# Kernel tuning notes

Measured on AMD Instinct MI355X. Metric: run time of the kernel, lower is better.

## Reference

```python
import jax, jax.numpy as jnp
import numpy as np

NUM_FEATURES = 256
NUM_PIDS = 5532
NUM_CQ = 5000
OIM_SCALAR = 30.0
IGNORE_INDEX = 5554  # roi_label 5555 -> label 5554 -> ignored by cross_entropy
N = 8192
UNLABELED_FRAC = 0.3


def _l2norm(x):
    return x / jnp.linalg.norm(x, axis=-1, keepdims=True)


def setup_inputs() -> dict:
    key = jax.random.key(0)
    k1, k2, k3, k4, k5 = jax.random.split(key, 5)
    inputs = _l2norm(jax.random.normal(k1, (N, NUM_FEATURES), dtype=jnp.float32))
    # roi_label values are 1..num_pids for labeled persons, 5555 for unlabeled;
    # all >= 1 so the `label >= 0` filter in the torch module keeps every row
    # (keeps shapes static / jit-friendly while matching the math exactly).
    labels = jax.random.randint(k2, (N,), 1, NUM_PIDS + 1, dtype=jnp.int32)
    unlabeled = jax.random.uniform(k3, (N,)) < UNLABELED_FRAC
    roi_label = jnp.where(unlabeled, IGNORE_INDEX + 1, labels).astype(jnp.int32)
    lut = _l2norm(jax.random.normal(k4, (NUM_PIDS, NUM_FEATURES), dtype=jnp.float32))
    cq = _l2norm(jax.random.normal(k5, (NUM_CQ, NUM_FEATURES), dtype=jnp.float32))
    return {"inputs": inputs, "roi_label": roi_label, "lut": lut, "cq": cq}


def reference(inputs, roi_label, lut, cq):
    # targets = cat(roi_label); label = targets - 1; inds = label >= 0 keeps all rows here
    label = roi_label - 1  # [N], values in [0, NUM_PIDS-1] or IGNORE_INDEX
    # OIMSMR.forward: projected = [inputs @ lut.T | inputs @ cq.T]
    logits = jnp.concatenate([inputs @ lut.T, inputs @ cq.T], axis=1)  # [N, P+Q]
    logits = logits * OIM_SCALAR
    # cross_entropy with ignore_index=5554 (mean over non-ignored samples)
    valid = label != IGNORE_INDEX
    safe_label = jnp.clip(label, 0, logits.shape[1] - 1)
    logp = jax.nn.log_softmax(logits, axis=1)  # [N, P+Q]
    nll = -jnp.take_along_axis(logp, safe_label[:, None], axis=1)[:, 0]  # [N]
    n_valid = jnp.maximum(jnp.sum(valid.astype(jnp.float32)), 1.0)
    loss = jnp.sum(jnp.where(valid, nll, 0.0)) / n_valid
    return loss
```

## Files before the change

kernel.cpp:

```cpp
#include <hip/hip_runtime.h>
#include <hip/hip_bf16.h>
#include <cstdint>
#include <cstddef>

#define N_ROWS 8192
#define K_DIM  256
#define NP     5532
#define NC     10532
#define NCPAD  10752
#define IGN    5554
#define BM     128
#define BN     128
#define BK     128
#define CT     84
#define NBLK   (CT * 64)
#define CPX    (NBLK / 8)
#define WSCALE 43.2808512266689f
#define LN2    0.69314718055994531f

#if __has_builtin(__builtin_amdgcn_exp2f)
#define EXP2F(x) __builtin_amdgcn_exp2f(x)
#else
#define EXP2F(x) __expf((x) * LN2)
#endif

using f32x4 = __attribute__((ext_vector_type(4))) float;
using i64x2 = __attribute__((ext_vector_type(2))) long;

__global__ __launch_bounds__(256) void oim_convert(
    const float* __restrict__ X, const float* __restrict__ lut,
    const float* __restrict__ cq,
    unsigned char* __restrict__ Xb, unsigned char* __restrict__ Wb)
{
    const int XCH = (N_ROWS * K_DIM) / 8;
    const int WCH = (NCPAD * K_DIM) / 8;
    int c = blockIdx.x * 256 + threadIdx.x;
    if (c >= XCH + WCH) return;
    const float* src = nullptr;
    unsigned char* dst;
    float scale = 1.0f;
    int row, qg;
    if (c < XCH) {
        row = c >> 5; qg = c & 31;
        src = X + (size_t)c * 8;
        dst = Xb + (size_t)row * K_DIM;
    } else {
        int wc = c - XCH;
        row = wc >> 5; qg = wc & 31;
        dst = Wb + (size_t)row * K_DIM;
        scale = WSCALE;
        if (row < NP)      src = lut + (size_t)row * K_DIM + qg * 8;
        else if (row < NC) src = cq + (size_t)(row - NP) * K_DIM + qg * 8;
    }
    dst += (qg >> 3) * 64 + (qg & 3) * 16 + ((qg >> 2) & 1) * 8;
    unsigned int lo = 0, hi = 0;
    if (src) {
        float4 v0 = *reinterpret_cast<const float4*>(src);
        float4 v1 = *reinterpret_cast<const float4*>(src + 4);
        lo = __builtin_amdgcn_cvt_pk_fp8_f32(v0.x * scale, v0.y * scale, 0,  false);
        lo = __builtin_amdgcn_cvt_pk_fp8_f32(v0.z * scale, v0.w * scale, lo, true);
        hi = __builtin_amdgcn_cvt_pk_fp8_f32(v1.x * scale, v1.y * scale, 0,  false);
        hi = __builtin_amdgcn_cvt_pk_fp8_f32(v1.z * scale, v1.w * scale, hi, true);
    }
    uint2 o; o.x = lo; o.y = hi;
    *reinterpret_cast<uint2*>(dst) = o;
}

__global__ __launch_bounds__(256, 3) void oim_gemm(
    const unsigned char* __restrict__ Xb, const unsigned char* __restrict__ Wb,
    const int* __restrict__ roi,
    float* __restrict__ partial, float* __restrict__ labelLogit)
{
    const int bid = blockIdx.x;
    const int L   = (bid & 7) * CPX + (bid >> 3);
    const int ct  = L >> 6;
    const int rt  = L & 63;
    const int row0 = rt * BM;
    const int col0 = ct * BN;
    const int tid  = threadIdx.x;
    const int wave = tid >> 6;
    const int lane = tid & 63;
    const int wm   = (wave >> 1) * 64;
    const int wn   = (wave & 1) * 64;

    __shared__ __align__(16) unsigned char As[BM * BK];
    __shared__ __align__(16) unsigned char Bs[BN * BK];
    __shared__ int   lbl[BM];
    __shared__ float rs[BM][2];

    if (tid < BM) lbl[tid] = roi[row0 + tid] - 1;

    const unsigned char* aP[4];
    const unsigned char* bP[4];
#pragma unroll
    for (int i = 0; i < 4; ++i) {
        int c = i * 256 + tid;
        int r = c >> 3;
        int u = c & 7;
        int s = ((u ^ (r & 7)) << 4);
        aP[i] = Xb + (size_t)(row0 + r) * K_DIM + s;
        bP[i] = Wb + (size_t)(col0 + r) * K_DIM + s;
    }

    const int rA = wm + (lane & 15);
    const int rB = wn + (lane & 15);
    const int gs = lane >> 4;
    int aO[2], bO[2];
#pragma unroll
    for (int kb = 0; kb < 2; ++kb) {
        aO[kb] = rA * 128 + (((kb * 4 + gs) ^ (rA & 7)) << 4);
        bO[kb] = rB * 128 + (((kb * 4 + gs) ^ (rB & 7)) << 4);
    }

    f32x4 acc[4][4] = {};
    long xa0[4], xa1[4], xb0[4], xb1[4];

    auto readfrag = [&](int kb) {
#pragma unroll
        for (int m = 0; m < 4; ++m) {
            i64x2 v = *reinterpret_cast<const i64x2*>(As + aO[kb] + m * 2048);
            xa0[m] = v.x; xa1[m] = v.y;
        }
#pragma unroll
        for (int n = 0; n < 4; ++n) {
            i64x2 v = *reinterpret_cast<const i64x2*>(Bs + bO[kb] + n * 2048);
            xb0[n] = v.x; xb1[n] = v.y;
        }
    };
    auto mfmafrag = [&]() {
#pragma unroll
        for (int m = 0; m < 4; ++m)
#pragma unroll
            for (int n = 0; n < 4; ++n)
                acc[m][n] = __builtin_amdgcn_mfma_f32_16x16x32_fp8_fp8(
                    xa0[m], xb0[n], acc[m][n], 0, 0, 0);
#pragma unroll
        for (int m = 0; m < 4; ++m)
#pragma unroll
            for (int n = 0; n < 4; ++n)
                acc[m][n] = __builtin_amdgcn_mfma_f32_16x16x32_fp8_fp8(
                    xa1[m], xb1[n], acc[m][n], 0, 0, 0);
    };

#define STAGE(T)                                                              \
    do {                                                                      \
        _Pragma("unroll")                                                     \
        for (int i = 0; i < 4; ++i) {                                         \
            __builtin_amdgcn_global_load_lds(                                 \
                (const __attribute__((address_space(1))) void*)aP[i],         \
                (__attribute__((address_space(3))) void*)                     \
                    ((char*)As + i * 4096 + wave * 1024), 16, (T) * 128, 0);  \
            __builtin_amdgcn_global_load_lds(                                 \
                (const __attribute__((address_space(1))) void*)bP[i],         \
                (__attribute__((address_space(3))) void*)                     \
                    ((char*)Bs + i * 4096 + wave * 1024), 16, (T) * 128, 0);  \
        }                                                                     \
    } while (0)

    STAGE(0);
    __syncthreads();

    readfrag(0); mfmafrag();
    readfrag(1);
    __syncthreads();
    STAGE(1);
    mfmafrag();
    __syncthreads();

    readfrag(0); mfmafrag();
    readfrag(1); mfmafrag();
#undef STAGE

#pragma unroll
    for (int m = 0; m < 4; ++m) {
#pragma unroll
        for (int reg = 0; reg < 4; ++reg) {
            int lrow = wm + m * 16 + (lane >> 4) * 4 + reg;
            int grow = row0 + lrow;
            int lab  = lbl[lrow];
            float s = 0.0f;
#pragma unroll
            for (int n = 0; n < 4; ++n) {
                int gcol = col0 + wn + n * 16 + (lane & 15);
                float a = acc[m][n][reg];
                s += EXP2F(a);
                if (gcol == lab) labelLogit[grow] = a;
            }
#pragma unroll
            for (int off = 1; off < 16; off <<= 1) s += __shfl_xor(s, off, 64);
            if ((lane & 15) == 0) rs[lrow][wave & 1] = s;
        }
    }
    __syncthreads();
    if (tid < BM)
        partial[(size_t)ct * N_ROWS + row0 + tid] = rs[tid][0] + rs[tid][1];
}

__global__ __launch_bounds__(256) void oim_rownll(
    const float* __restrict__ partial, const float* __restrict__ labelLogit,
    const int* __restrict__ roi, float* __restrict__ blksum)
{
    __shared__ float s1[256], s2[256];
    int tid = threadIdx.x;
    int r = blockIdx.x * 256 + tid;
    float S = 0.0f;
    for (int t = 0; t < CT; ++t) S += partial[(size_t)t * N_ROWS + r];
    float lse = logf(S);
    int lab = roi[r] - 1;
    bool valid = (lab != IGN);
    s1[tid] = valid ? (lse - labelLogit[r] * LN2) : 0.0f;
    s2[tid] = valid ? 1.0f : 0.0f;
    __syncthreads();
    for (int o = 128; o > 0; o >>= 1) {
        if (tid < o) { s1[tid] += s1[tid + o]; s2[tid] += s2[tid + o]; }
        __syncthreads();
    }
    if (tid == 0) {
        blksum[blockIdx.x]      = s1[0];
        blksum[32 + blockIdx.x] = s2[0];
    }
}

__global__ __launch_bounds__(64) void oim_reduce(
    const float* __restrict__ blksum, float* __restrict__ out)
{
    int tid = threadIdx.x;
    float a = (tid < 32) ? blksum[tid]      : 0.0f;
    float b = (tid < 32) ? blksum[32 + tid] : 0.0f;
#pragma unroll
    for (int off = 32; off > 0; off >>= 1) {
        a += __shfl_xor(a, off, 64);
        b += __shfl_xor(b, off, 64);
    }
    if (tid == 0) out[0] = a / fmaxf(b, 1.0f);
}

extern "C" void kernel_launch(void* const* d_in, const int* in_sizes, int n_in,
                              void* d_out, int out_size, void* d_ws, size_t ws_size,
                              hipStream_t stream)
{
    const float* X   = (const float*)d_in[0];
    const int*   roi = (const int*)  d_in[1];
    const float* lut = (const float*)d_in[2];
    const float* cq  = (const float*)d_in[3];
    float* out = (float*)d_out;

    char* ws = (char*)d_ws;
    unsigned char* Xb = (unsigned char*)ws;
    unsigned char* Wb = Xb + (size_t)N_ROWS * K_DIM;
    float* partial    = (float*)(Wb + (size_t)NCPAD * K_DIM);
    float* labelLogit = partial + (size_t)CT * N_ROWS;
    float* blksum     = labelLogit + N_ROWS;
    size_t need = (size_t)N_ROWS * K_DIM + (size_t)NCPAD * K_DIM
                + (size_t)CT * N_ROWS * 4 + (size_t)(N_ROWS + 64) * 4;
    if (ws_size < need) return;

    const int TOT_CHUNKS = ((N_ROWS + NCPAD) * K_DIM) / 8;
    oim_convert<<<(TOT_CHUNKS + 255) / 256, 256, 0, stream>>>(X, lut, cq, Xb, Wb);
    oim_gemm<<<NBLK, 256, 0, stream>>>(Xb, Wb, roi, partial, labelLogit);
    oim_rownll<<<N_ROWS / 256, 256, 0, stream>>>(partial, labelLogit, roi, blksum);
    oim_reduce<<<1, 64, 0, stream>>>(blksum, out);
}
```

Baseline: 63.17 us.

## Load full K=256 tile into LDS at once instead of two K-halves

New measurement: 84.69 us. 34.1% more time.

```diff
diff --git a/kernel.cpp b/kernel.cpp
--- a/kernel.cpp
+++ b/kernel.cpp
@@ -11,7 +11,6 @@
 #define IGN    5554
 #define BM     128
 #define BN     128
-#define BK     128
 #define CT     84
 #define NBLK   (CT * 64)
 #define CPX    (NBLK / 8)
@@ -66,7 +65,7 @@
     *reinterpret_cast<uint2*>(dst) = o;
 }
 
-__global__ __launch_bounds__(256, 3) void oim_gemm(
+__global__ __launch_bounds__(256, 2) void oim_gemm(
     const unsigned char* __restrict__ Xb, const unsigned char* __restrict__ Wb,
     const int* __restrict__ roi,
     float* __restrict__ partial, float* __restrict__ labelLogit)
@@ -83,51 +82,56 @@
     const int wm   = (wave >> 1) * 64;
     const int wn   = (wave & 1) * 64;
 
-    __shared__ __align__(16) unsigned char As[BM * BK];
-    __shared__ __align__(16) unsigned char Bs[BN * BK];
+    __shared__ __align__(16) unsigned char As[BM * K_DIM];
+    __shared__ __align__(16) unsigned char Bs[BN * K_DIM];
     __shared__ int   lbl[BM];
     __shared__ float rs[BM][2];
 
     if (tid < BM) lbl[tid] = roi[row0 + tid] - 1;
 
-    const unsigned char* aP[4];
-    const unsigned char* bP[4];
-#pragma unroll
-    for (int i = 0; i < 4; ++i) {
-        int c = i * 256 + tid;
-        int r = c >> 3;
-        int u = c & 7;
-        int s = ((u ^ (r & 7)) << 4);
-        aP[i] = Xb + (size_t)(row0 + r) * K_DIM + s;
-        bP[i] = Wb + (size_t)(col0 + r) * K_DIM + s;
-    }
+    const int r0 = tid >> 4;
+    const int ug = (tid & 15) ^ r0;
+    const unsigned char* aS = Xb + (size_t)(row0 + r0) * K_DIM + (ug << 4);
+    const unsigned char* bS = Wb + (size_t)(col0 + r0) * K_DIM + (ug << 4);
+
+#pragma unroll
+    for (int i = 0; i < 8; ++i) {
+        __builtin_amdgcn_global_load_lds(
+            (const __attribute__((address_space(1))) void*)(aS + i * 4096),
+            (__attribute__((address_space(3))) void*)
+                ((char*)As + i * 4096 + tid * 16), 16, 0, 0);
+        __builtin_amdgcn_global_load_lds(
+            (const __attribute__((address_space(1))) void*)(bS + i * 4096),
+            (__attribute__((address_space(3))) void*)
+                ((char*)Bs + i * 4096 + tid * 16), 16, 0, 0);
+    }
+    __syncthreads();
 
     const int rA = wm + (lane & 15);
     const int rB = wn + (lane & 15);
     const int gs = lane >> 4;
-    int aO[2], bO[2];
-#pragma unroll
-    for (int kb = 0; kb < 2; ++kb) {
-        aO[kb] = rA * 128 + (((kb * 4 + gs) ^ (rA & 7)) << 4);
-        bO[kb] = rB * 128 + (((kb * 4 + gs) ^ (rB & 7)) << 4);
+    int aO[4], bO[4];
+#pragma unroll
+    for (int kb = 0; kb < 4; ++kb) {
+        aO[kb] = rA * 256 + (((kb * 4 + gs) ^ (rA & 15)) << 4);
+        bO[kb] = rB * 256 + (((kb * 4 + gs) ^ (rB & 15)) << 4);
     }
 
     f32x4 acc[4][4] = {};
-    long xa0[4], xa1[4], xb0[4], xb1[4];
-
-    auto readfrag = [&](int kb) {
+
+#pragma unroll
+    for (int kb = 0; kb < 4; ++kb) {
+        long xa0[4], xa1[4], xb0[4], xb1[4];
 #pragma unroll
         for (int m = 0; m < 4; ++m) {
-            i64x2 v = *reinterpret_cast<const i64x2*>(As + aO[kb] + m * 2048);
+            i64x2 v = *reinterpret_cast<const i64x2*>(As + aO[kb] + m * 4096);
             xa0[m] = v.x; xa1[m] = v.y;
         }
 #pragma unroll
         for (int n = 0; n < 4; ++n) {
-            i64x2 v = *reinterpret_cast<const i64x2*>(Bs + bO[kb] + n * 2048);
+            i64x2 v = *reinterpret_cast<const i64x2*>(Bs + bO[kb] + n * 4096);
             xb0[n] = v.x; xb1[n] = v.y;
         }
-    };
-    auto mfmafrag = [&]() {
 #pragma unroll
         for (int m = 0; m < 4; ++m)
 #pragma unroll
@@ -140,36 +144,7 @@
             for (int n = 0; n < 4; ++n)
                 acc[m][n] = __builtin_amdgcn_mfma_f32_16x16x32_fp8_fp8(
                     xa1[m], xb1[n], acc[m][n], 0, 0, 0);
-    };
-
-#define STAGE(T)                                                              \
-    do {                                                                      \
-        _Pragma("unroll")                                                     \
-        for (int i = 0; i < 4; ++i) {                                         \
-            __builtin_amdgcn_global_load_lds(                                 \
-                (const __attribute__((address_space(1))) void*)aP[i],         \
-                (__attribute__((address_space(3))) void*)                     \
-                    ((char*)As + i * 4096 + wave * 1024), 16, (T) * 128, 0);  \
-            __builtin_amdgcn_global_load_lds(                                 \
-                (const __attribute__((address_space(1))) void*)bP[i],         \
-                (__attribute__((address_space(3))) void*)                     \
-                    ((char*)Bs + i * 4096 + wave * 1024), 16, (T) * 128, 0);  \
-        }                                                                     \
-    } while (0)
-
-    STAGE(0);
-    __syncthreads();
-
-    readfrag(0); mfmafrag();
-    readfrag(1);
-    __syncthreads();
-    STAGE(1);
-    mfmafrag();
-    __syncthreads();
-
-    readfrag(0); mfmafrag();
-    readfrag(1); mfmafrag();
-#undef STAGE
+    }
 
 #pragma unroll
     for (int m = 0; m < 4; ++m) {
```

## Use scaled 16x16x128 FP8 MFMA instead of 16x16x32 FP8 MFMA

Applied to the files above, without the earlier changes.

Result: slower. 67.89 us (+7.5%).

```diff
diff --git a/kernel.cpp b/kernel.cpp
--- a/kernel.cpp
+++ b/kernel.cpp
@@ -17,6 +17,7 @@
 #define CPX    (NBLK / 8)
 #define WSCALE 43.2808512266689f
 #define LN2    0.69314718055994531f
+#define SC1    0x7F7F7F7F
 
 #if __has_builtin(__builtin_amdgcn_exp2f)
 #define EXP2F(x) __builtin_amdgcn_exp2f(x)
@@ -25,7 +26,8 @@
 #endif
 
 using f32x4 = __attribute__((ext_vector_type(4))) float;
-using i64x2 = __attribute__((ext_vector_type(2))) long;
+using i32x4 = __attribute__((ext_vector_type(4))) int;
+using i32x8 = __attribute__((ext_vector_type(8))) int;
 
 __global__ __launch_bounds__(256) void oim_convert(
     const float* __restrict__ X, const float* __restrict__ lut,
@@ -39,20 +41,18 @@
     const float* src = nullptr;
     unsigned char* dst;
     float scale = 1.0f;
-    int row, qg;
     if (c < XCH) {
-        row = c >> 5; qg = c & 31;
         src = X + (size_t)c * 8;
-        dst = Xb + (size_t)row * K_DIM;
+        dst = Xb + (size_t)c * 8;
     } else {
-        int wc = c - XCH;
-        row = wc >> 5; qg = wc & 31;
-        dst = Wb + (size_t)row * K_DIM;
+        int wc  = c - XCH;
+        int row = wc >> 5;
+        int off = (wc & 31) * 8;
+        dst = Wb + (size_t)wc * 8;
         scale = WSCALE;
-        if (row < NP)      src = lut + (size_t)row * K_DIM + qg * 8;
-        else if (row < NC) src = cq + (size_t)(row - NP) * K_DIM + qg * 8;
-    }
-    dst += (qg >> 3) * 64 + (qg & 3) * 16 + ((qg >> 2) & 1) * 8;
+        if (row < NP)      src = lut + (size_t)row * K_DIM + off;
+        else if (row < NC) src = cq + (size_t)(row - NP) * K_DIM + off;
+    }
     unsigned int lo = 0, hi = 0;
     if (src) {
         float4 v0 = *reinterpret_cast<const float4*>(src);
@@ -105,41 +105,38 @@
     const int rA = wm + (lane & 15);
     const int rB = wn + (lane & 15);
     const int gs = lane >> 4;
-    int aO[2], bO[2];
-#pragma unroll
-    for (int kb = 0; kb < 2; ++kb) {
-        aO[kb] = rA * 128 + (((kb * 4 + gs) ^ (rA & 7)) << 4);
-        bO[kb] = rB * 128 + (((kb * 4 + gs) ^ (rB & 7)) << 4);
-    }
+    const int aO0 = rA * 128 + (((2 * gs)     ^ (rA & 7)) << 4);
+    const int aO1 = rA * 128 + (((2 * gs + 1) ^ (rA & 7)) << 4);
+    const int bO0 = rB * 128 + (((2 * gs)     ^ (rB & 7)) << 4);
+    const int bO1 = rB * 128 + (((2 * gs + 1) ^ (rB & 7)) << 4);
 
     f32x4 acc[4][4] = {};
-    long xa0[4], xa1[4], xb0[4], xb1[4];
-
-    auto readfrag = [&](int kb) {
+    i32x8 av[4], bv[4];
+
+    auto readfrag = [&]() {
 #pragma unroll
         for (int m = 0; m < 4; ++m) {
-            i64x2 v = *reinterpret_cast<const i64x2*>(As + aO[kb] + m * 2048);
-            xa0[m] = v.x; xa1[m] = v.y;
+            i32x4 lo = *reinterpret_cast<const i32x4*>(As + aO0 + m * 2048);
+            i32x4 hi = *reinterpret_cast<const i32x4*>(As + aO1 + m * 2048);
+            av[m] = __builtin_shufflevector(lo, hi, 0, 1, 2, 3, 4, 5, 6, 7);
         }
 #pragma unroll
         for (int n = 0; n < 4; ++n) {
-            i64x2 v = *reinterpret_cast<const i64x2*>(Bs + bO[kb] + n * 2048);
-            xb0[n] = v.x; xb1[n] = v.y;
+            i32x4 lo = *reinterpret_cast<const i32x4*>(Bs + bO0 + n * 2048);
+            i32x4 hi = *reinterpret_cast<const i32x4*>(Bs + bO1 + n * 2048);
+            bv[n] = __builtin_shufflevector(lo, hi, 0, 1, 2, 3, 4, 5, 6, 7);
         }
     };
-    auto mfmafrag = [&]() {
+    auto mfmaall = [&]() {
 #pragma unroll
         for (int m = 0; m < 4; ++m)
 #pragma unroll
             for (int n = 0; n < 4; ++n)
-                acc[m][n] = __builtin_amdgcn_mfma_f32_16x16x32_fp8_fp8(
-                    xa0[m], xb0[n], acc[m][n], 0, 0, 0);
-#pragma unroll
-        for (int m = 0; m < 4; ++m)
-#pragma unroll
-            for (int n = 0; n < 4; ++n)
-                acc[m][n] = __builtin_amdgcn_mfma_f32_16x16x32_fp8_fp8(
-                    xa1[m], xb1[n], acc[m][n], 0, 0, 0);
+                acc[m][n] = __builtin_amdgcn_mfma_scale_f32_16x16x128_f8f6f4(
+                    av[m], bv[n], acc[m][n],
+                    0, 0,
+                    0, SC1,
+                    0, SC1);
     };
 
 #define STAGE(T)                                                              \
@@ -160,15 +157,14 @@
     STAGE(0);
     __syncthreads();
 
-    readfrag(0); mfmafrag();
-    readfrag(1);
+    readfrag();
     __syncthreads();
     STAGE(1);
-    mfmafrag();
-    __syncthreads();
-
-    readfrag(0); mfmafrag();
-    readfrag(1); mfmafrag();
+    mfmaall();
+    __syncthreads();
+
+    readfrag();
+    mfmaall();
 #undef STAGE
 
 #pragma unroll
```
